# Kernel tuning notes

Measured on AMD Instinct MI355X. Metric: run time of the kernel, lower is better.

## Reference

```python
import jax, jax.numpy as jnp
import numpy as np

H = 64        # hidden_dim
A = 21        # N_ACTIONS
B = 262144    # batch size


def setup_inputs() -> dict:
    key = jax.random.key(0)
    ks = jax.random.split(key, 32)

    def w(k, shape):
        fan_in = shape[0]
        return (jax.random.normal(k, shape, jnp.float32) / np.float32(np.sqrt(fan_in)))

    inp = {
        "x": jax.random.normal(ks[0], (B, 2, 2), jnp.float32),
        "b_act1": jax.random.randint(ks[1], (B,), 0, A),
        "b_act2": jax.random.randint(ks[2], (B,), 0, A),
        # enc: Linear(2,H), ReLU, Linear(H,H), ReLU
        "enc_w1": w(ks[3], (2, H)), "enc_b1": jnp.zeros((H,), jnp.float32),
        "enc_w2": w(ks[4], (H, H)), "enc_b2": jnp.zeros((H,), jnp.float32),
        # q_net: Linear(H,H), ReLU, Linear(H,A)
        "q_w1": w(ks[5], (H, H)), "q_b1": jnp.zeros((H,), jnp.float32),
        "q_w2": w(ks[6], (H, A)), "q_b2": jnp.zeros((A,), jnp.float32),
        # v_net: Linear(H,H), ReLU, Linear(H,1)
        "v_w1": w(ks[7], (H, H)), "v_b1": jnp.zeros((H,), jnp.float32),
        "v_w2": w(ks[8], (H, 1)), "v_b2": jnp.zeros((1,), jnp.float32),
        # lin2: Linear(H+A,H), ReLU, Linear(H,H), ReLU, Linear(H,H)
        "l2_w1": w(ks[9], (H + A, H)), "l2_b1": jnp.zeros((H,), jnp.float32),
        "l2_w2": w(ks[10], (H, H)), "l2_b2": jnp.zeros((H,), jnp.float32),
        "l2_w3": w(ks[11], (H, H)), "l2_b3": jnp.zeros((H,), jnp.float32),
        # lin3, lin4
        "l3_w": w(ks[12], (H, H)), "l3_b": jnp.zeros((H,), jnp.float32),
        "l4_w": w(ks[13], (H, A)), "l4_b": jnp.zeros((A,), jnp.float32),
        # q_prime_net: Linear(H,2H) ELU Linear(2H,H) ELU Linear(H,H) ELU Linear(H,1)
        "qp_w1": w(ks[14], (H, 2 * H)), "qp_b1": jnp.zeros((2 * H,), jnp.float32),
        "qp_w2": w(ks[15], (2 * H, H)), "qp_b2": jnp.zeros((H,), jnp.float32),
        "qp_w3": w(ks[16], (H, H)), "qp_b3": jnp.zeros((H,), jnp.float32),
        "qp_w4": w(ks[17], (H, 1)), "qp_b4": jnp.zeros((1,), jnp.float32),
    }
    return inp


def reference(x, b_act1, b_act2,
              enc_w1, enc_b1, enc_w2, enc_b2,
              q_w1, q_b1, q_w2, q_b2,
              v_w1, v_b1, v_w2, v_b2,
              l2_w1, l2_b1, l2_w2, l2_b2, l2_w3, l2_b3,
              l3_w, l3_b, l4_w, l4_b,
              qp_w1, qp_b1, qp_w2, qp_b2, qp_w3, qp_b3, qp_w4, qp_b4):
    relu = jax.nn.relu
    elu = jax.nn.elu

    def enc(z):
        return relu(relu(z @ enc_w1 + enc_b1) @ enc_w2 + enc_b2)

    def q_net(h):
        return relu(h @ q_w1 + q_b1) @ q_w2 + q_b2

    def lin2(e):  # ends with bare Linear (no final activation)
        h = relu(e @ l2_w1 + l2_b1)
        h = relu(h @ l2_w2 + l2_b2)
        return h @ l2_w3 + l2_b3

    def q_prime(z):
        h = elu(z @ qp_w1 + qp_b1)
        h = elu(h @ qp_w2 + qp_b2)
        h = elu(h @ qp_w3 + qp_b3)
        return h @ qp_w4 + qp_b4

    h1 = enc(x[:, 0, :])  # [B,H]
    h2 = enc(x[:, 1, :])
    q1, q2 = q_net(h1), q_net(h2)              # [B,A]
    key2 = jnp.stack([h1, h2], axis=1)          # [B,2,H]
    vtot = relu((h1 + h2) @ v_w1 + v_b1) @ v_w2 + v_b2  # [B,1]

    def joint(act1, act2):
        oh1 = jax.nn.one_hot(act1, A, dtype=h1.dtype)
        oh2 = jax.nn.one_hot(act2, A, dtype=h2.dtype)
        e = jnp.stack([jnp.concatenate([h1, oh1], axis=-1),
                       jnp.concatenate([h2, oh2], axis=-1)], axis=1)  # [B,2,H+A]
        key1 = lin2(e)                              # [B,2,H]
        q = q_prime(key1.mean(axis=1))              # [B,1]
        return key1, q

    key1, joint_qs = joint(b_act1, b_act2)
    a1_max = jnp.argmax(q1, axis=1)
    a2_max = jnp.argmax(q2, axis=1)
    key1_max, joint_max_qs = joint(a1_max, a2_max)

    def q_jt(k1):
        z = key2 + k1.mean(axis=1, keepdims=True) - k1 / 2  # [B,2,H]
        return relu(z @ l3_w + l3_b) @ l4_w + l4_b           # [B,2,A]

    q_jt_alt = q_jt(key1)
    q_jt_max_alt = q_jt(key1_max)

    return (q1, q2, joint_qs, joint_max_qs, vtot, q_jt_alt, q_jt_max_alt)
```

## Files before the change

kernel.cpp:

```cpp
#include <hip/hip_runtime.h>
#include <hip/hip_bf16.h>


#define B_TOT 262144

typedef __bf16 bf16_t;
typedef __bf16 bf16x8 __attribute__((ext_vector_type(8)));
typedef float  f32x4  __attribute__((ext_vector_type(4)));

#define MFMA16(a, b, c) __builtin_amdgcn_mfma_f32_16x16x32_bf16((a), (b), (c), 0, 0, 0)
#define LDS_SYNC() __builtin_amdgcn_fence(__ATOMIC_SEQ_CST, "workgroup")

enum : int {
  OFF_VW1  = 0,
  OFF_L2W1 = 4096,
  OFF_L2W2 = 8192,
  OFF_L2W3 = 12288,
  OFF_L3W  = 16384,
  OFF_L4W  = 20480,
  OFF_QP1  = 22528,
  OFF_QP2  = 30720,
  OFF_QP3  = 38912,
  WS_ELEMS = 43008
};
#define WS_BYTES (WS_ELEMS * 2)

enum : int {
  O_Q1   = 0,
  O_Q2   = 21 * B_TOT,
  O_JQ   = 42 * B_TOT,
  O_JMQ  = 43 * B_TOT,
  O_VT   = 44 * B_TOT,
  O_QJT  = 45 * B_TOT,
  O_QJTM = 87 * B_TOT
};

struct RDesc { const float* src; int K; int N; int NT; int off; };
struct RPack { RDesc d[9]; };

__global__ void repack_kernel(RPack P, bf16_t* __restrict__ ws) {
  RDesc d = P.d[blockIdx.x];
  int n = (d.K >> 5) * d.NT * 512;
  for (int i = threadIdx.x; i < n; i += blockDim.x) {
    int j  = i & 7;
    int l  = (i >> 3) & 63;
    int t  = i >> 9;
    int nt = t % d.NT;
    int kc = t / d.NT;
    int sk = kc * 32 + ((l >> 4) << 3) + j;
    int sn = nt * 16 + (l & 15);
    float v = (sn < d.N) ? d.src[sk * d.N + sn] : 0.0f;
    ws[d.off + i] = (bf16_t)v;
  }
}

struct Args {
  const float* x; const int* a1; const int* a2;
  const float* ew1; const float* eb1; const float* ew2; const float* eb2;
  const float* qw1; const float* qb1; const float* qw2; const float* qb2;
  const float* vw1; const float* vb1; const float* vw2; const float* vb2;
  const float* l2w1; const float* l2b1; const float* l2w2; const float* l2b2;
  const float* l2w3; const float* l2b3;
  const float* l3w;  const float* l3b;  const float* l4w;  const float* l4b;
  const float* qpw1; const float* qpb1; const float* qpw2; const float* qpb2;
  const float* qpw3; const float* qpb3; const float* qpw4; const float* qpb4;
  float* out; const bf16_t* ws;
};

struct __align__(16) SMem {
  bf16_t h1b[64 * 72];
  bf16_t h2b[64 * 72];
  unsigned char scr[35840];
  bf16_t oneh[21 * 64];
  float  bias[768];
  int    acts[128];
  int    amax[128];
  float  red[64][2];
  int    redi[64][2];
};

__device__ __forceinline__ float eluf(float x) { return x > 0.f ? x : expm1f(x); }

__device__ __forceinline__ void fcA64(const float* __restrict__ fin, float* __restrict__ fout,
                                      const float* __restrict__ W, const float* __restrict__ Bv,
                                      bf16_t* hb, int r, int g) {
  float2 acc[8];
#pragma unroll
  for (int i = 0; i < 8; i++) acc[i] = make_float2(Bv[g * 16 + 2 * i], Bv[g * 16 + 2 * i + 1]);
#pragma unroll 4
  for (int k4 = 0; k4 < 16; k4++) {
    float4 a = *(const float4*)(fin + r * 68 + k4 * 4);
    float av[4] = {a.x, a.y, a.z, a.w};
#pragma unroll
    for (int kk = 0; kk < 4; kk++) {
      const float2* wr = (const float2*)(W + (k4 * 4 + kk) * 64 + g * 16);
#pragma unroll
      for (int i = 0; i < 8; i++) {
        float2 w = wr[i];
        acc[i].x = fmaf(av[kk], w.x, acc[i].x);
        acc[i].y = fmaf(av[kk], w.y, acc[i].y);
      }
    }
  }
#pragma unroll
  for (int i = 0; i < 8; i++) {
    float v0 = fmaxf(acc[i].x, 0.f), v1 = fmaxf(acc[i].y, 0.f);
    fout[r * 68 + g * 16 + 2 * i]     = v0;
    fout[r * 68 + g * 16 + 2 * i + 1] = v1;
    if (hb) {
      hb[r * 72 + g * 16 + 2 * i]     = (bf16_t)v0;
      hb[r * 72 + g * 16 + 2 * i + 1] = (bf16_t)v1;
    }
  }
}

template <int NC>
__device__ __forceinline__ void qn2(const float* __restrict__ fin, const float* __restrict__ W21,
                                    const float* __restrict__ Bv, float* __restrict__ qo,
                                    int r, int colbase, float& bv, int& bi) {
  float acc[NC];
#pragma unroll
  for (int i = 0; i < NC; i++) acc[i] = Bv[colbase + i];
  for (int k4 = 0; k4 < 16; k4++) {
    float4 a = *(const float4*)(fin + r * 68 + k4 * 4);
    float av[4] = {a.x, a.y, a.z, a.w};
#pragma unroll
    for (int kk = 0; kk < 4; kk++) {
      const float* wr = W21 + (k4 * 4 + kk) * 21 + colbase;
#pragma unroll
      for (int i = 0; i < NC; i++) acc[i] = fmaf(av[kk], wr[i], acc[i]);
    }
  }
  bv = -3e38f; bi = 0;
#pragma unroll
  for (int i = 0; i < NC; i++) {
    qo[i] = acc[i];
    if (acc[i] > bv) { bv = acc[i]; bi = colbase + i; }
  }
}

template <bool USEWS>
__global__ __launch_bounds__(256) void qtran_main(Args A) {
  __shared__ SMem sm;
  const int t = threadIdx.x;
  const int wgbase = blockIdx.x * 64;
  const int r = t & 63;
  const int g = __builtin_amdgcn_readfirstlane(t >> 6);

  float* f0 = (float*)sm.scr;
  float* f1 = f0 + 64 * 68;

  if (t < 64) {
    sm.bias[t]        = A.vb1[t];
    sm.bias[64 + t]   = A.l2b1[t];
    sm.bias[128 + t]  = A.l2b2[t];
    sm.bias[192 + t]  = A.l2b3[t];
    sm.bias[384 + t]  = A.qpb2[t];
    sm.bias[448 + t]  = A.qpb3[t];
    sm.bias[512 + t]  = A.l3b[t];
    sm.bias[608 + t]  = A.vw2[t];
    sm.bias[672 + t]  = A.qpw4[t];
    sm.acts[t]        = A.a1[wgbase + t];
    sm.acts[64 + t]   = A.a2[wgbase + t];
  } else if (t < 192) {
    sm.bias[256 + t - 64] = A.qpb1[t - 64];
  } else if (t < 224) {
    int i = t - 192;
    sm.bias[576 + i] = (i < 21) ? A.l4b[i] : 0.0f;
  } else if (t == 224) {
    sm.bias[736] = A.vb2[0];
    sm.bias[737] = A.qpb4[0];
  }
  for (int i = t; i < 21 * 64; i += 256)
    sm.oneh[i] = (bf16_t)A.l2w1[(64 + (i >> 6)) * 64 + (i & 63)];

  const int rowg = wgbase + r;
  float4 xv = ((const float4*)A.x)[rowg];
#pragma unroll 1
  for (int s = 0; s < 2; ++s) {
    float xa = s ? xv.z : xv.x;
    float xb = s ? xv.w : xv.y;
#pragma unroll
    for (int cc = 0; cc < 16; cc++) {
      int col = g * 16 + cc;
      float h = fmaf(xa, A.ew1[col], fmaf(xb, A.ew1[64 + col], A.eb1[col]));
      f0[r * 68 + col] = fmaxf(h, 0.f);
    }
    __syncthreads();
    fcA64(f0, f1, A.ew2, A.eb2, s ? sm.h2b : sm.h1b, r, g);
    __syncthreads();
    fcA64(f1, f0, A.qw1, A.qb1, nullptr, r, g);
    __syncthreads();
    {
      float* qo = A.out + (s ? O_Q2 : O_Q1) + rowg * 21;
      float bv; int bi;
      if (g == 0) {
        qn2<16>(f0, A.qw2, A.qb2, qo, r, 0, bv, bi);
        sm.red[r][0] = bv; sm.redi[r][0] = bi;
      } else if (g == 1) {
        qn2<5>(f0, A.qw2, A.qb2, qo + 16, r, 16, bv, bi);
        sm.red[r][1] = bv; sm.redi[r][1] = bi;
      }
    }
    __syncthreads();
    if (t < 64)
      sm.amax[s * 64 + t] = (sm.red[t][0] >= sm.red[t][1]) ? sm.redi[t][0] : sm.redi[t][1];
    __syncthreads();
  }
  __syncthreads();

  const int l = t & 63, c = l & 15, q = l >> 4;
  const int rb = g * 16;
  bf16_t* st = (bf16_t*)sm.scr;
  bf16_t* k1 = st + 64 * 136;
  float* out = A.out;
  const bf16x8* WF = (const bf16x8*)A.ws;

  auto BF = [&](const float* __restrict__ Wp, int N, int woff, int kc, int nt, int NT) -> bf16x8 {
    if constexpr (USEWS) {
      (void)Wp; (void)N;
      return WF[(woff >> 3) + (kc * NT + nt) * 64 + l];
    } else {
      (void)woff;
      int sk = kc * 32 + q * 8, sn = nt * 16 + c;
      bf16x8 v;
      if (sn < N) {
#pragma unroll
        for (int j = 0; j < 8; j++) v[j] = (bf16_t)Wp[(sk + j) * N + sn];
      } else {
#pragma unroll
        for (int j = 0; j < 8; j++) v[j] = (bf16_t)0.0f;
      }
      return v;
    }
  };
  auto AF = [&](const bf16_t* buf, int stride, int row, int ko) -> bf16x8 {
    return *(const bf16x8*)(buf + row * stride + ko);
  };

  {
    bf16x8 aS[2];
#pragma unroll
    for (int kc = 0; kc < 2; kc++) {
      bf16x8 u = AF(sm.h1b, 72, rb + c, kc * 32 + q * 8);
      bf16x8 v = AF(sm.h2b, 72, rb + c, kc * 32 + q * 8);
      bf16x8 s8;
#pragma unroll
      for (int i = 0; i < 8; i++) s8[i] = (bf16_t)((float)u[i] + (float)v[i]);
      aS[kc] = s8;
    }
    float pr[4] = {};
#pragma unroll
    for (int nt = 0; nt < 4; nt++) {
      bf16x8 b0 = BF(A.vw1, 64, OFF_VW1, 0, nt, 4), b1 = BF(A.vw1, 64, OFF_VW1, 1, nt, 4);
      float bb = sm.bias[nt * 16 + c];
      float wv = sm.bias[608 + nt * 16 + c];
      f32x4 acc = {bb, bb, bb, bb};
      acc = MFMA16(aS[0], b0, acc);
      acc = MFMA16(aS[1], b1, acc);
#pragma unroll
      for (int rI = 0; rI < 4; rI++) pr[rI] += fmaxf(acc[rI], 0.f) * wv;
    }
#pragma unroll
    for (int rI = 0; rI < 4; rI++) {
      float v = pr[rI];
      v += __shfl_xor(v, 1, 64);
      v += __shfl_xor(v, 2, 64);
      v += __shfl_xor(v, 4, 64);
      v += __shfl_xor(v, 8, 64);
      if (c == 0)
        out[O_VT + wgbase + rb + q * 4 + rI] = v + sm.bias[736];
    }
  }

  auto J = [&](const int* av1, const int* av2, int jointBase, int qjtBase) {
    LDS_SYNC();
#pragma unroll 1
    for (int j = 0; j < 2; j++) {
      const bf16_t* HB = j ? sm.h2b : sm.h1b;
      const int* av = j ? av2 : av1;
      int act[4];
#pragma unroll
      for (int rI = 0; rI < 4; rI++) act[rI] = av[rb + q * 4 + rI];
      bf16x8 aF0 = AF(HB, 72, rb + c, q * 8);
      bf16x8 aF1 = AF(HB, 72, rb + c, 32 + q * 8);
#pragma unroll
      for (int nt = 0; nt < 4; nt++) {
        bf16x8 b0 = BF(A.l2w1, 64, OFF_L2W1, 0, nt, 4), b1 = BF(A.l2w1, 64, OFF_L2W1, 1, nt, 4);
        float bb = sm.bias[64 + nt * 16 + c];
        f32x4 acc = {bb, bb, bb, bb};
        acc = MFMA16(aF0, b0, acc);
        acc = MFMA16(aF1, b1, acc);
#pragma unroll
        for (int rI = 0; rI < 4; rI++) {
          float v = acc[rI] + (float)sm.oneh[act[rI] * 64 + nt * 16 + c];
          st[(rb + q * 4 + rI) * 136 + nt * 16 + c] = (bf16_t)fmaxf(v, 0.f);
        }
      }
      LDS_SYNC();
      aF0 = AF(st, 136, rb + c, q * 8);
      aF1 = AF(st, 136, rb + c, 32 + q * 8);
      LDS_SYNC();
#pragma unroll
      for (int nt = 0; nt < 4; nt++) {
        bf16x8 b0 = BF(A.l2w2, 64, OFF_L2W2, 0, nt, 4), b1 = BF(A.l2w2, 64, OFF_L2W2, 1, nt, 4);
        float bb = sm.bias[128 + nt * 16 + c];
        f32x4 acc = {bb, bb, bb, bb};
        acc = MFMA16(aF0, b0, acc);
        acc = MFMA16(aF1, b1, acc);
#pragma unroll
        for (int rI = 0; rI < 4; rI++)
          st[(rb + q * 4 + rI) * 136 + nt * 16 + c] = (bf16_t)fmaxf(acc[rI], 0.f);
      }
      LDS_SYNC();
      aF0 = AF(st, 136, rb + c, q * 8);
      aF1 = AF(st, 136, rb + c, 32 + q * 8);
      LDS_SYNC();
#pragma unroll
      for (int nt = 0; nt < 4; nt++) {
        bf16x8 b0 = BF(A.l2w3, 64, OFF_L2W3, 0, nt, 4), b1 = BF(A.l2w3, 64, OFF_L2W3, 1, nt, 4);
        float bb = sm.bias[192 + nt * 16 + c];
        f32x4 acc = {bb, bb, bb, bb};
        acc = MFMA16(aF0, b0, acc);
        acc = MFMA16(aF1, b1, acc);
#pragma unroll
        for (int rI = 0; rI < 4; rI++)
          k1[(rb + q * 4 + rI) * 144 + j * 72 + nt * 16 + c] = (bf16_t)acc[rI];
      }
      LDS_SYNC();
    }
    bf16x8 aM[2];
#pragma unroll
    for (int kc = 0; kc < 2; kc++) {
      bf16x8 u = AF(k1, 144, rb + c, kc * 32 + q * 8);
      bf16x8 v = AF(k1, 144, rb + c, 72 + kc * 32 + q * 8);
      bf16x8 m;
#pragma unroll
      for (int i = 0; i < 8; i++) m[i] = (bf16_t)(0.5f * ((float)u[i] + (float)v[i]));
      aM[kc] = m;
    }
#pragma unroll
    for (int nt = 0; nt < 8; nt++) {
      bf16x8 b0 = BF(A.qpw1, 128, OFF_QP1, 0, nt, 8), b1 = BF(A.qpw1, 128, OFF_QP1, 1, nt, 8);
      float bb = sm.bias[256 + nt * 16 + c];
      f32x4 acc = {bb, bb, bb, bb};
      acc = MFMA16(aM[0], b0, acc);
      acc = MFMA16(aM[1], b1, acc);
#pragma unroll
      for (int rI = 0; rI < 4; rI++)
        st[(rb + q * 4 + rI) * 136 + nt * 16 + c] = (bf16_t)eluf(acc[rI]);
    }
    LDS_SYNC();
    {
      bf16x8 aQ[4];
#pragma unroll
      for (int kc = 0; kc < 4; kc++) aQ[kc] = AF(st, 136, rb + c, kc * 32 + q * 8);
      LDS_SYNC();
#pragma unroll
      for (int nt = 0; nt < 4; nt++) {
        bf16x8 bq0 = BF(A.qpw2, 64, OFF_QP2, 0, nt, 4), bq1 = BF(A.qpw2, 64, OFF_QP2, 1, nt, 4);
        bf16x8 bq2 = BF(A.qpw2, 64, OFF_QP2, 2, nt, 4), bq3 = BF(A.qpw2, 64, OFF_QP2, 3, nt, 4);
        float bb = sm.bias[384 + nt * 16 + c];
        f32x4 acc = {bb, bb, bb, bb};
        acc = MFMA16(aQ[0], bq0, acc);
        acc = MFMA16(aQ[1], bq1, acc);
        acc = MFMA16(aQ[2], bq2, acc);
        acc = MFMA16(aQ[3], bq3, acc);
#pragma unroll
        for (int rI = 0; rI < 4; rI++)
          st[(rb + q * 4 + rI) * 136 + nt * 16 + c] = (bf16_t)eluf(acc[rI]);
      }
    }
    LDS_SYNC();
    {
      bf16x8 aP0 = AF(st, 136, rb + c, q * 8);
      bf16x8 aP1 = AF(st, 136, rb + c, 32 + q * 8);
      float pj[4] = {};
#pragma unroll
      for (int nt = 0; nt < 4; nt++) {
        bf16x8 b0 = BF(A.qpw3, 64, OFF_QP3, 0, nt, 4), b1 = BF(A.qpw3, 64, OFF_QP3, 1, nt, 4);
        float bb = sm.bias[448 + nt * 16 + c];
        float w4 = sm.bias[672 + nt * 16 + c];
        f32x4 acc = {bb, bb, bb, bb};
        acc = MFMA16(aP0, b0, acc);
        acc = MFMA16(aP1, b1, acc);
#pragma unroll
        for (int rI = 0; rI < 4; rI++) pj[rI] += eluf(acc[rI]) * w4;
      }
#pragma unroll
      for (int rI = 0; rI < 4; rI++) {
        float v = pj[rI];
        v += __shfl_xor(v, 1, 64);
        v += __shfl_xor(v, 2, 64);
        v += __shfl_xor(v, 4, 64);
        v += __shfl_xor(v, 8, 64);
        if (c == 0)
          out[jointBase + wgbase + rb + q * 4 + rI] = v + sm.bias[737];
      }
    }
#pragma unroll 1
    for (int j = 0; j < 2; j++) {
      LDS_SYNC();
      const bf16_t* HB = j ? sm.h2b : sm.h1b;
      bf16x8 aZ[2];
#pragma unroll
      for (int kc = 0; kc < 2; kc++) {
        bf16x8 u  = AF(HB, 72, rb + c, kc * 32 + q * 8);
        bf16x8 kk = AF(k1, 144, rb + c, (1 - j) * 72 + kc * 32 + q * 8);
        bf16x8 z;
#pragma unroll
        for (int i = 0; i < 8; i++) z[i] = (bf16_t)((float)u[i] + 0.5f * (float)kk[i]);
        aZ[kc] = z;
      }
#pragma unroll
      for (int nt = 0; nt < 4; nt++) {
        bf16x8 b0 = BF(A.l3w, 64, OFF_L3W, 0, nt, 4), b1 = BF(A.l3w, 64, OFF_L3W, 1, nt, 4);
        float bb = sm.bias[512 + nt * 16 + c];
        f32x4 acc = {bb, bb, bb, bb};
        acc = MFMA16(aZ[0], b0, acc);
        acc = MFMA16(aZ[1], b1, acc);
#pragma unroll
        for (int rI = 0; rI < 4; rI++)
          st[(rb + q * 4 + rI) * 136 + nt * 16 + c] = (bf16_t)fmaxf(acc[rI], 0.f);
      }
      LDS_SYNC();
      bf16x8 aL0 = AF(st, 136, rb + c, q * 8);
      bf16x8 aL1 = AF(st, 136, rb + c, 32 + q * 8);
#pragma unroll
      for (int nt = 0; nt < 2; nt++) {
        bf16x8 b0 = BF(A.l4w, 21, OFF_L4W, 0, nt, 2), b1 = BF(A.l4w, 21, OFF_L4W, 1, nt, 2);
        float bb = sm.bias[576 + nt * 16 + c];
        int col = nt * 16 + c;
        f32x4 acc = {bb, bb, bb, bb};
        acc = MFMA16(aL0, b0, acc);
        acc = MFMA16(aL1, b1, acc);
        if (col < 21) {
#pragma unroll
          for (int rI = 0; rI < 4; rI++)
            out[qjtBase + (wgbase + rb + q * 4 + rI) * 42 + j * 21 + col] = acc[rI];
        }
      }
    }
  };

  J(sm.acts, sm.acts + 64, O_JQ, O_QJT);
  J(sm.amax, sm.amax + 64, O_JMQ, O_QJTM);
}

extern "C" void kernel_launch(void* const* d_in, const int* in_sizes, int n_in,
                              void* d_out, int out_size, void* d_ws, size_t ws_size,
                              hipStream_t stream) {
  (void)in_sizes; (void)n_in; (void)out_size;
  Args A;
  A.x    = (const float*)d_in[0];
  A.a1   = (const int*)d_in[1];
  A.a2   = (const int*)d_in[2];
  A.ew1  = (const float*)d_in[3];
  A.eb1  = (const float*)d_in[4];
  A.ew2  = (const float*)d_in[5];
  A.eb2  = (const float*)d_in[6];
  A.qw1  = (const float*)d_in[7];
  A.qb1  = (const float*)d_in[8];
  A.qw2  = (const float*)d_in[9];
  A.qb2  = (const float*)d_in[10];
  A.vw1  = (const float*)d_in[11];
  A.vb1  = (const float*)d_in[12];
  A.vw2  = (const float*)d_in[13];
  A.vb2  = (const float*)d_in[14];
  A.l2w1 = (const float*)d_in[15];
  A.l2b1 = (const float*)d_in[16];
  A.l2w2 = (const float*)d_in[17];
  A.l2b2 = (const float*)d_in[18];
  A.l2w3 = (const float*)d_in[19];
  A.l2b3 = (const float*)d_in[20];
  A.l3w  = (const float*)d_in[21];
  A.l3b  = (const float*)d_in[22];
  A.l4w  = (const float*)d_in[23];
  A.l4b  = (const float*)d_in[24];
  A.qpw1 = (const float*)d_in[25];
  A.qpb1 = (const float*)d_in[26];
  A.qpw2 = (const float*)d_in[27];
  A.qpb2 = (const float*)d_in[28];
  A.qpw3 = (const float*)d_in[29];
  A.qpb3 = (const float*)d_in[30];
  A.qpw4 = (const float*)d_in[31];
  A.qpb4 = (const float*)d_in[32];
  A.out  = (float*)d_out;
  A.ws   = (const bf16_t*)d_ws;

  if (ws_size >= (size_t)WS_BYTES) {
    bf16_t* ws = (bf16_t*)d_ws;
    RPack P;
    P.d[0] = {A.vw1,  64, 64,  4, OFF_VW1};
    P.d[1] = {A.l2w1, 64, 64,  4, OFF_L2W1};
    P.d[2] = {A.l2w2, 64, 64,  4, OFF_L2W2};
    P.d[3] = {A.l2w3, 64, 64,  4, OFF_L2W3};
    P.d[4] = {A.l3w,  64, 64,  4, OFF_L3W};
    P.d[5] = {A.l4w,  64, 21,  2, OFF_L4W};
    P.d[6] = {A.qpw1, 64, 128, 8, OFF_QP1};
    P.d[7] = {A.qpw2, 128, 64, 4, OFF_QP2};
    P.d[8] = {A.qpw3, 64, 64,  4, OFF_QP3};
    hipLaunchKernelGGL(repack_kernel, dim3(9), dim3(256), 0, stream, P, ws);
    hipLaunchKernelGGL(HIP_KERNEL_NAME(qtran_main<true>), dim3(B_TOT / 64), dim3(256), 0,
                       stream, A);
  } else {
    hipLaunchKernelGGL(HIP_KERNEL_NAME(qtran_main<false>), dim3(B_TOT / 64), dim3(256), 0,
                       stream, A);
  }
}
```

Before: 935.7 us.

## Chain MLP layers in registers via transposed MFMA, removing LDS round-trips

Swaps MFMA operand roles so weights are the A operand and activations the B operand, and permutes the packed weight layout so each layer's accumulator output maps directly onto the next layer's B-fragment. Intermediate activations stay in registers instead of being written to and reread from LDS between layers, and the k1 mean is kept as fp32 register sums. This removes many LDS stores, loads and fences, at the cost of higher register pressure. The launch bounds now request two workgroups per CU, which may cause spills.

```diff
diff --git a/kernel.cpp b/kernel.cpp
--- a/kernel.cpp
+++ b/kernel.cpp
@@ -5,11 +5,11 @@
 #define B_TOT 262144
 
 typedef __bf16 bf16_t;
+typedef __bf16 bf16x4 __attribute__((ext_vector_type(4)));
 typedef __bf16 bf16x8 __attribute__((ext_vector_type(8)));
 typedef float  f32x4  __attribute__((ext_vector_type(4)));
 
 #define MFMA16(a, b, c) __builtin_amdgcn_mfma_f32_16x16x32_bf16((a), (b), (c), 0, 0, 0)
-#define LDS_SYNC() __builtin_amdgcn_fence(__ATOMIC_SEQ_CST, "workgroup")
 
 enum : int {
   OFF_VW1  = 0,
@@ -47,7 +47,7 @@
     int t  = i >> 9;
     int nt = t % d.NT;
     int kc = t / d.NT;
-    int sk = kc * 32 + ((l >> 4) << 3) + j;
+    int sk = kc * 32 + 16 * (j >> 2) + 4 * (l >> 4) + (j & 3);
     int sn = nt * 16 + (l & 15);
     float v = (sn < d.N) ? d.src[sk * d.N + sn] : 0.0f;
     ws[d.off + i] = (bf16_t)v;
@@ -70,9 +70,9 @@
 struct __align__(16) SMem {
   bf16_t h1b[64 * 72];
   bf16_t h2b[64 * 72];
-  unsigned char scr[35840];
-  bf16_t oneh[21 * 64];
+  unsigned char scr[34816];
   float  bias[768];
+  bf16_t oneh[21 * 68];
   int    acts[128];
   int    amax[128];
   float  red[64][2];
@@ -139,8 +139,53 @@
   }
 }
 
+template <bool USEWS, int NT, int KC>
+__device__ __forceinline__ void layerT(const bf16x8* __restrict__ WF,
+                                       const float* __restrict__ Wp, int N, int woff,
+                                       const bf16x8* __restrict__ bin,
+                                       const float* __restrict__ bias, int bbase,
+                                       int l, int c, int u, f32x4* __restrict__ acc) {
+#pragma unroll
+  for (int nt = 0; nt < NT; nt++) {
+    f32x4 a = *(const f32x4*)(bias + bbase + nt * 16 + 4 * u);
+#pragma unroll
+    for (int kc = 0; kc < KC; kc++) {
+      bf16x8 w;
+      if constexpr (USEWS) {
+        w = WF[(woff >> 3) + (kc * NT + nt) * 64 + l];
+      } else {
+        int sn = nt * 16 + c;
+        if (sn < N) {
+#pragma unroll
+          for (int j = 0; j < 8; j++)
+            w[j] = (bf16_t)Wp[(kc * 32 + 16 * (j >> 2) + 4 * u + (j & 3)) * N + sn];
+        } else {
+#pragma unroll
+          for (int j = 0; j < 8; j++) w[j] = (bf16_t)0.0f;
+        }
+      }
+      a = MFMA16(w, bin[kc], a);
+    }
+    acc[nt] = a;
+  }
+}
+
+template <int MODE, int NKC>
+__device__ __forceinline__ void packT(const f32x4* __restrict__ acc,
+                                      bf16x8* __restrict__ bout) {
+#pragma unroll
+  for (int kc = 0; kc < NKC; kc++)
+#pragma unroll
+    for (int j = 0; j < 8; j++) {
+      float v = acc[2 * kc + (j >> 2)][j & 3];
+      if constexpr (MODE == 1) v = fmaxf(v, 0.f);
+      if constexpr (MODE == 2) v = eluf(v);
+      bout[kc][j] = (bf16_t)v;
+    }
+}
+
 template <bool USEWS>
-__global__ __launch_bounds__(256) void qtran_main(Args A) {
+__global__ __launch_bounds__(256, 2) void qtran_main(Args A) {
   __shared__ SMem sm;
   const int t = threadIdx.x;
   const int wgbase = blockIdx.x * 64;
@@ -171,8 +216,10 @@
     sm.bias[736] = A.vb2[0];
     sm.bias[737] = A.qpb4[0];
   }
-  for (int i = t; i < 21 * 64; i += 256)
-    sm.oneh[i] = (bf16_t)A.l2w1[(64 + (i >> 6)) * 64 + (i & 63)];
+  for (int i = t; i < 21 * 68; i += 256) {
+    int a_ = i / 68, n_ = i % 68;
+    sm.oneh[i] = (bf16_t)((n_ < 64) ? A.l2w1[(64 + a_) * 64 + n_] : 0.0f);
+  }
 
   const int rowg = wgbase + r;
   float4 xv = ((const float4*)A.x)[rowg];
@@ -209,237 +256,129 @@
   }
   __syncthreads();
 
-  const int l = t & 63, c = l & 15, q = l >> 4;
+  const int l = t & 63;
+  const int c = l & 15, u = l >> 4;
   const int rb = g * 16;
-  bf16_t* st = (bf16_t*)sm.scr;
-  bf16_t* k1 = st + 64 * 136;
+  const int row = rb + c;
   float* out = A.out;
   const bf16x8* WF = (const bf16x8*)A.ws;
-
-  auto BF = [&](const float* __restrict__ Wp, int N, int woff, int kc, int nt, int NT) -> bf16x8 {
-    if constexpr (USEWS) {
-      (void)Wp; (void)N;
-      return WF[(woff >> 3) + (kc * NT + nt) * 64 + l];
-    } else {
-      (void)woff;
-      int sk = kc * 32 + q * 8, sn = nt * 16 + c;
-      bf16x8 v;
-      if (sn < N) {
-#pragma unroll
-        for (int j = 0; j < 8; j++) v[j] = (bf16_t)Wp[(sk + j) * N + sn];
-      } else {
-#pragma unroll
-        for (int j = 0; j < 8; j++) v[j] = (bf16_t)0.0f;
-      }
-      return v;
-    }
-  };
-  auto AF = [&](const bf16_t* buf, int stride, int row, int ko) -> bf16x8 {
-    return *(const bf16x8*)(buf + row * stride + ko);
+  const float* bias = sm.bias;
+
+  auto HG = [&](const bf16_t* __restrict__ HB, int kc) -> bf16x8 {
+    const bf16_t* p = HB + row * 72 + kc * 32 + 4 * u;
+    bf16x4 lo = *(const bf16x4*)p;
+    bf16x4 hi = *(const bf16x4*)(p + 16);
+    bf16x8 rr;
+#pragma unroll
+    for (int d = 0; d < 4; d++) { rr[d] = lo[d]; rr[4 + d] = hi[d]; }
+    return rr;
   };
 
   {
     bf16x8 aS[2];
 #pragma unroll
     for (int kc = 0; kc < 2; kc++) {
-      bf16x8 u = AF(sm.h1b, 72, rb + c, kc * 32 + q * 8);
-      bf16x8 v = AF(sm.h2b, 72, rb + c, kc * 32 + q * 8);
+      bf16x8 a1 = HG(sm.h1b, kc), a2 = HG(sm.h2b, kc);
       bf16x8 s8;
 #pragma unroll
-      for (int i = 0; i < 8; i++) s8[i] = (bf16_t)((float)u[i] + (float)v[i]);
+      for (int i = 0; i < 8; i++) s8[i] = (bf16_t)((float)a1[i] + (float)a2[i]);
       aS[kc] = s8;
     }
-    float pr[4] = {};
+    f32x4 acc[4];
+    layerT<USEWS, 4, 2>(WF, A.vw1, 64, OFF_VW1, aS, bias, 0, l, c, u, acc);
+    float pr = 0.f;
 #pragma unroll
     for (int nt = 0; nt < 4; nt++) {
-      bf16x8 b0 = BF(A.vw1, 64, OFF_VW1, 0, nt, 4), b1 = BF(A.vw1, 64, OFF_VW1, 1, nt, 4);
-      float bb = sm.bias[nt * 16 + c];
-      float wv = sm.bias[608 + nt * 16 + c];
-      f32x4 acc = {bb, bb, bb, bb};
-      acc = MFMA16(aS[0], b0, acc);
-      acc = MFMA16(aS[1], b1, acc);
-#pragma unroll
-      for (int rI = 0; rI < 4; rI++) pr[rI] += fmaxf(acc[rI], 0.f) * wv;
-    }
-#pragma unroll
-    for (int rI = 0; rI < 4; rI++) {
-      float v = pr[rI];
-      v += __shfl_xor(v, 1, 64);
-      v += __shfl_xor(v, 2, 64);
-      v += __shfl_xor(v, 4, 64);
-      v += __shfl_xor(v, 8, 64);
-      if (c == 0)
-        out[O_VT + wgbase + rb + q * 4 + rI] = v + sm.bias[736];
-    }
-  }
-
-  auto J = [&](const int* av1, const int* av2, int jointBase, int qjtBase) {
-    LDS_SYNC();
-#pragma unroll 1
+      f32x4 wv = *(const f32x4*)(bias + 608 + nt * 16 + 4 * u);
+#pragma unroll
+      for (int p = 0; p < 4; p++) pr += fmaxf(acc[nt][p], 0.f) * wv[p];
+    }
+    pr += __shfl_xor(pr, 16, 64);
+    pr += __shfl_xor(pr, 32, 64);
+    if (u == 0) out[O_VT + wgbase + row] = pr + bias[736];
+  }
+
+  auto J = [&](const int* __restrict__ av1, const int* __restrict__ av2,
+               int jointBase, int qjtBase) {
+    bf16x8 k1f[2][2];
+    f32x4 msum[4];
+#pragma unroll
     for (int j = 0; j < 2; j++) {
       const bf16_t* HB = j ? sm.h2b : sm.h1b;
-      const int* av = j ? av2 : av1;
-      int act[4];
-#pragma unroll
-      for (int rI = 0; rI < 4; rI++) act[rI] = av[rb + q * 4 + rI];
-      bf16x8 aF0 = AF(HB, 72, rb + c, q * 8);
-      bf16x8 aF1 = AF(HB, 72, rb + c, 32 + q * 8);
+      const int act = (j ? av2 : av1)[row];
+      bf16x8 bh[2];
+#pragma unroll
+      for (int kc = 0; kc < 2; kc++) bh[kc] = HG(HB, kc);
+      f32x4 acc[4];
+      layerT<USEWS, 4, 2>(WF, A.l2w1, 64, OFF_L2W1, bh, bias, 64, l, c, u, acc);
 #pragma unroll
       for (int nt = 0; nt < 4; nt++) {
-        bf16x8 b0 = BF(A.l2w1, 64, OFF_L2W1, 0, nt, 4), b1 = BF(A.l2w1, 64, OFF_L2W1, 1, nt, 4);
-        float bb = sm.bias[64 + nt * 16 + c];
-        f32x4 acc = {bb, bb, bb, bb};
-        acc = MFMA16(aF0, b0, acc);
-        acc = MFMA16(aF1, b1, acc);
-#pragma unroll
-        for (int rI = 0; rI < 4; rI++) {
-          float v = acc[rI] + (float)sm.oneh[act[rI] * 64 + nt * 16 + c];
-          st[(rb + q * 4 + rI) * 136 + nt * 16 + c] = (bf16_t)fmaxf(v, 0.f);
-        }
+        bf16x4 oh = *(const bf16x4*)(sm.oneh + act * 68 + nt * 16 + 4 * u);
+#pragma unroll
+        for (int p = 0; p < 4; p++) acc[nt][p] += (float)oh[p];
       }
-      LDS_SYNC();
-      aF0 = AF(st, 136, rb + c, q * 8);
-      aF1 = AF(st, 136, rb + c, 32 + q * 8);
-      LDS_SYNC();
-#pragma unroll
-      for (int nt = 0; nt < 4; nt++) {
-        bf16x8 b0 = BF(A.l2w2, 64, OFF_L2W2, 0, nt, 4), b1 = BF(A.l2w2, 64, OFF_L2W2, 1, nt, 4);
-        float bb = sm.bias[128 + nt * 16 + c];
-        f32x4 acc = {bb, bb, bb, bb};
-        acc = MFMA16(aF0, b0, acc);
-        acc = MFMA16(aF1, b1, acc);
-#pragma unroll
-        for (int rI = 0; rI < 4; rI++)
-          st[(rb + q * 4 + rI) * 136 + nt * 16 + c] = (bf16_t)fmaxf(acc[rI], 0.f);
-      }
-      LDS_SYNC();
-      aF0 = AF(st, 136, rb + c, q * 8);
-      aF1 = AF(st, 136, rb + c, 32 + q * 8);
-      LDS_SYNC();
-#pragma unroll
-      for (int nt = 0; nt < 4; nt++) {
-        bf16x8 b0 = BF(A.l2w3, 64, OFF_L2W3, 0, nt, 4), b1 = BF(A.l2w3, 64, OFF_L2W3, 1, nt, 4);
-        float bb = sm.bias[192 + nt * 16 + c];
-        f32x4 acc = {bb, bb, bb, bb};
-        acc = MFMA16(aF0, b0, acc);
-        acc = MFMA16(aF1, b1, acc);
-#pragma unroll
-        for (int rI = 0; rI < 4; rI++)
-          k1[(rb + q * 4 + rI) * 144 + j * 72 + nt * 16 + c] = (bf16_t)acc[rI];
-      }
-      LDS_SYNC();
+      bf16x8 b1[2];
+      packT<1, 2>(acc, b1);
+      layerT<USEWS, 4, 2>(WF, A.l2w2, 64, OFF_L2W2, b1, bias, 128, l, c, u, acc);
+      bf16x8 b2[2];
+      packT<1, 2>(acc, b2);
+      layerT<USEWS, 4, 2>(WF, A.l2w3, 64, OFF_L2W3, b2, bias, 192, l, c, u, acc);
+      packT<0, 2>(acc, k1f[j]);
+#pragma unroll
+      for (int nt = 0; nt < 4; nt++)
+        msum[nt] = j ? (msum[nt] + acc[nt]) : acc[nt];
     }
     bf16x8 aM[2];
 #pragma unroll
-    for (int kc = 0; kc < 2; kc++) {
-      bf16x8 u = AF(k1, 144, rb + c, kc * 32 + q * 8);
-      bf16x8 v = AF(k1, 144, rb + c, 72 + kc * 32 + q * 8);
-      bf16x8 m;
-#pragma unroll
-      for (int i = 0; i < 8; i++) m[i] = (bf16_t)(0.5f * ((float)u[i] + (float)v[i]));
-      aM[kc] = m;
-    }
-#pragma unroll
-    for (int nt = 0; nt < 8; nt++) {
-      bf16x8 b0 = BF(A.qpw1, 128, OFF_QP1, 0, nt, 8), b1 = BF(A.qpw1, 128, OFF_QP1, 1, nt, 8);
-      float bb = sm.bias[256 + nt * 16 + c];
-      f32x4 acc = {bb, bb, bb, bb};
-      acc = MFMA16(aM[0], b0, acc);
-      acc = MFMA16(aM[1], b1, acc);
-#pragma unroll
-      for (int rI = 0; rI < 4; rI++)
-        st[(rb + q * 4 + rI) * 136 + nt * 16 + c] = (bf16_t)eluf(acc[rI]);
-    }
-    LDS_SYNC();
-    {
-      bf16x8 aQ[4];
-#pragma unroll
-      for (int kc = 0; kc < 4; kc++) aQ[kc] = AF(st, 136, rb + c, kc * 32 + q * 8);
-      LDS_SYNC();
-#pragma unroll
-      for (int nt = 0; nt < 4; nt++) {
-        bf16x8 bq0 = BF(A.qpw2, 64, OFF_QP2, 0, nt, 4), bq1 = BF(A.qpw2, 64, OFF_QP2, 1, nt, 4);
-        bf16x8 bq2 = BF(A.qpw2, 64, OFF_QP2, 2, nt, 4), bq3 = BF(A.qpw2, 64, OFF_QP2, 3, nt, 4);
-        float bb = sm.bias[384 + nt * 16 + c];
-        f32x4 acc = {bb, bb, bb, bb};
-        acc = MFMA16(aQ[0], bq0, acc);
-        acc = MFMA16(aQ[1], bq1, acc);
-        acc = MFMA16(aQ[2], bq2, acc);
-        acc = MFMA16(aQ[3], bq3, acc);
-#pragma unroll
-        for (int rI = 0; rI < 4; rI++)
-          st[(rb + q * 4 + rI) * 136 + nt * 16 + c] = (bf16_t)eluf(acc[rI]);
-      }
-    }
-    LDS_SYNC();
-    {
-      bf16x8 aP0 = AF(st, 136, rb + c, q * 8);
-      bf16x8 aP1 = AF(st, 136, rb + c, 32 + q * 8);
-      float pj[4] = {};
-#pragma unroll
-      for (int nt = 0; nt < 4; nt++) {
-        bf16x8 b0 = BF(A.qpw3, 64, OFF_QP3, 0, nt, 4), b1 = BF(A.qpw3, 64, OFF_QP3, 1, nt, 4);
-        float bb = sm.bias[448 + nt * 16 + c];
-        float w4 = sm.bias[672 + nt * 16 + c];
-        f32x4 acc = {bb, bb, bb, bb};
-        acc = MFMA16(aP0, b0, acc);
-        acc = MFMA16(aP1, b1, acc);
-#pragma unroll
-        for (int rI = 0; rI < 4; rI++) pj[rI] += eluf(acc[rI]) * w4;
-      }
-#pragma unroll
-      for (int rI = 0; rI < 4; rI++) {
-        float v = pj[rI];
-        v += __shfl_xor(v, 1, 64);
-        v += __shfl_xor(v, 2, 64);
-        v += __shfl_xor(v, 4, 64);
-        v += __shfl_xor(v, 8, 64);
-        if (c == 0)
-          out[jointBase + wgbase + rb + q * 4 + rI] = v + sm.bias[737];
-      }
-    }
-#pragma unroll 1
+    for (int kc = 0; kc < 2; kc++)
+#pragma unroll
+      for (int j8 = 0; j8 < 8; j8++)
+        aM[kc][j8] = (bf16_t)(0.5f * msum[2 * kc + (j8 >> 2)][j8 & 3]);
+    f32x4 a8[8];
+    layerT<USEWS, 8, 2>(WF, A.qpw1, 128, OFF_QP1, aM, bias, 256, l, c, u, a8);
+    bf16x8 bq[4];
+    packT<2, 4>(a8, bq);
+    f32x4 acc[4];
+    layerT<USEWS, 4, 4>(WF, A.qpw2, 64, OFF_QP2, bq, bias, 384, l, c, u, acc);
+    bf16x8 b3[2];
+    packT<2, 2>(acc, b3);
+    layerT<USEWS, 4, 2>(WF, A.qpw3, 64, OFF_QP3, b3, bias, 448, l, c, u, acc);
+    float pj = 0.f;
+#pragma unroll
+    for (int nt = 0; nt < 4; nt++) {
+      f32x4 w4 = *(const f32x4*)(bias + 672 + nt * 16 + 4 * u);
+#pragma unroll
+      for (int p = 0; p < 4; p++) pj += eluf(acc[nt][p]) * w4[p];
+    }
+    pj += __shfl_xor(pj, 16, 64);
+    pj += __shfl_xor(pj, 32, 64);
+    if (u == 0) out[jointBase + wgbase + row] = pj + bias[737];
+#pragma unroll
     for (int j = 0; j < 2; j++) {
-      LDS_SYNC();
       const bf16_t* HB = j ? sm.h2b : sm.h1b;
       bf16x8 aZ[2];
 #pragma unroll
       for (int kc = 0; kc < 2; kc++) {
-        bf16x8 u  = AF(HB, 72, rb + c, kc * 32 + q * 8);
-        bf16x8 kk = AF(k1, 144, rb + c, (1 - j) * 72 + kc * 32 + q * 8);
-        bf16x8 z;
-#pragma unroll
-        for (int i = 0; i < 8; i++) z[i] = (bf16_t)((float)u[i] + 0.5f * (float)kk[i]);
-        aZ[kc] = z;
+        bf16x8 h8 = HG(HB, kc);
+        bf16x8 kk = k1f[1 - j][kc];
+#pragma unroll
+        for (int i = 0; i < 8; i++)
+          aZ[kc][i] = (bf16_t)((float)h8[i] + 0.5f * (float)kk[i]);
       }
-#pragma unroll
-      for (int nt = 0; nt < 4; nt++) {
-        bf16x8 b0 = BF(A.l3w, 64, OFF_L3W, 0, nt, 4), b1 = BF(A.l3w, 64, OFF_L3W, 1, nt, 4);
-        float bb = sm.bias[512 + nt * 16 + c];
-        f32x4 acc = {bb, bb, bb, bb};
-        acc = MFMA16(aZ[0], b0, acc);
-        acc = MFMA16(aZ[1], b1, acc);
-#pragma unroll
-        for (int rI = 0; rI < 4; rI++)
-          st[(rb + q * 4 + rI) * 136 + nt * 16 + c] = (bf16_t)fmaxf(acc[rI], 0.f);
-      }
-      LDS_SYNC();
-      bf16x8 aL0 = AF(st, 136, rb + c, q * 8);
-      bf16x8 aL1 = AF(st, 136, rb + c, 32 + q * 8);
-#pragma unroll
-      for (int nt = 0; nt < 2; nt++) {
-        bf16x8 b0 = BF(A.l4w, 21, OFF_L4W, 0, nt, 2), b1 = BF(A.l4w, 21, OFF_L4W, 1, nt, 2);
-        float bb = sm.bias[576 + nt * 16 + c];
-        int col = nt * 16 + c;
-        f32x4 acc = {bb, bb, bb, bb};
-        acc = MFMA16(aL0, b0, acc);
-        acc = MFMA16(aL1, b1, acc);
-        if (col < 21) {
-#pragma unroll
-          for (int rI = 0; rI < 4; rI++)
-            out[qjtBase + (wgbase + rb + q * 4 + rI) * 42 + j * 21 + col] = acc[rI];
+      f32x4 az[4];
+      layerT<USEWS, 4, 2>(WF, A.l3w, 64, OFF_L3W, aZ, bias, 512, l, c, u, az);
+      bf16x8 bz[2];
+      packT<1, 2>(az, bz);
+      f32x4 q2t[2];
+      layerT<USEWS, 2, 2>(WF, A.l4w, 21, OFF_L4W, bz, bias, 576, l, c, u, q2t);
+      const int ob = qjtBase + (wgbase + row) * 42 + j * 21;
+#pragma unroll
+      for (int nt = 0; nt < 2; nt++)
+#pragma unroll
+        for (int p = 0; p < 4; p++) {
+          int n2 = nt * 16 + 4 * u + p;
+          if (n2 < 21) out[ob + n2] = q2t[nt][p];
         }
-      }
     }
   };
 
```

Result: slower. 1.158 ms (+23.7%).
